# Optimization experiments

Hardware: AMD Instinct MI355X
Metric: run time of the kernel (lower is better)

The kernel has to match this reference:

```python
import jax, jax.numpy as jnp
import numpy as np

N_NODES = 50000
N_EDGES = 800000
D_IN = 256
D_OUT = 128


def setup_inputs() -> dict:
    key = jax.random.key(0)
    k1, k2, k3 = jax.random.split(key, 3)
    x = jax.random.normal(k1, (N_NODES, D_IN), dtype=jnp.float32)
    edge_index = jax.random.randint(k2, (2, N_EDGES), 0, N_NODES, dtype=jnp.int64)
    W = jax.random.normal(k3, (D_IN, D_OUT), dtype=jnp.float32) / np.sqrt(D_IN)
    b = jnp.zeros((D_OUT,), dtype=jnp.float32)
    prelu_a = jnp.full((D_OUT,), 0.25, dtype=jnp.float32)  # PyTorch PReLU default init
    return {"x": x, "edge_index": edge_index, "W": W, "b": b, "prelu_a": prelu_a}


def reference(x, edge_index, W, b, prelu_a):
    N = x.shape[0]
    # GCNConv default: add self-loops, symmetric deg^{-1/2} normalization
    self_loops = jnp.arange(N, dtype=edge_index.dtype)
    src = jnp.concatenate([edge_index[0], self_loops])  # message source j
    dst = jnp.concatenate([edge_index[1], self_loops])  # aggregation target i
    deg = jax.ops.segment_sum(jnp.ones_like(dst, dtype=x.dtype), dst, num_segments=N)
    dinv = jnp.where(deg > 0, jax.lax.rsqrt(deg), 0.0)
    norm = dinv[src] * dinv[dst]  # [E+N]
    h = x @ W  # [N, D_OUT] linear transform before aggregation
    msg = h[src] * norm[:, None]  # gather + scale
    out = jax.ops.segment_sum(msg, dst, num_segments=N) + b  # scatter-add + bias
    # per-channel PReLU
    return jnp.where(out > 0, out, prelu_a * out)
```

## Files before the change

kernel.cpp:

```cpp
#include <hip/hip_runtime.h>

#define N_NODES 50000
#define N_EDGES 800000
#define D_IN    256
#define D_OUT   128
#define ELL_S   64
#define GEMM_BLKS ((N_NODES + 127) / 128)
#define BKT_BLKS  ((N_EDGES + 1023) / 1024)
#define CNT_PAD   50176

typedef __attribute__((ext_vector_type(8))) short short8;
typedef __attribute__((ext_vector_type(4))) float floatx4;

__device__ __forceinline__ unsigned short f2bf(float f) {
    unsigned int u = __float_as_uint(f);
    unsigned int r = (u + 0x7fffu + ((u >> 16) & 1u)) >> 16;
    return (unsigned short)r;
}
__device__ __forceinline__ unsigned int pack2(float a, float b) {
    return (unsigned int)f2bf(a) | ((unsigned int)f2bf(b) << 16);
}
__device__ __forceinline__ float bfl(unsigned int u) { return __uint_as_float(u << 16); }
__device__ __forceinline__ float bfh(unsigned int u) { return __uint_as_float(u & 0xffff0000u); }

__device__ __forceinline__ int load_idx(const void* ei, int i, int is64) {
    if (is64) return (int)((const long long*)ei)[i];
    return ((const int*)ei)[i];
}

__global__ __launch_bounds__(256) void prep_kernel(const unsigned int* __restrict__ e,
                                                   int* __restrict__ is64,
                                                   const float* __restrict__ W,
                                                   unsigned short* __restrict__ bf,
                                                   int* __restrict__ cnt) {
    int bid = blockIdx.x;
    int tid = threadIdx.x;
    if (bid == 0) {
        __shared__ int found32;
        if (tid == 0) found32 = 0;
        __syncthreads();
        for (int i = tid; i < 2048; i += 256)
            if (e[2 * i + 1] != 0u) found32 = 1;
        __syncthreads();
        if (tid == 0) *is64 = (found32 ? 0 : 1);
    } else if (bid <= 16) {
        int g = (bid - 1) * 256 + tid;
        int lane = g & 63;
        int kc   = (g >> 6) & 7;
        int ct   = g >> 9;
        int n  = ct * 16 + (lane & 15);
        int kb = kc * 32 + ((lane >> 4) & 3) * 8;
        unsigned int p[4];
#pragma unroll
        for (int jj = 0; jj < 4; jj++) {
            float a = W[(size_t)(kb + 2 * jj + 0) * D_OUT + n];
            float b = W[(size_t)(kb + 2 * jj + 1) * D_OUT + n];
            p[jj] = pack2(a, b);
        }
        *(uint4*)&bf[(size_t)g * 8] = make_uint4(p[0], p[1], p[2], p[3]);
    } else {
        int i0 = ((bid - 17) * 256 + tid) * 2;
        *(int2*)&cnt[i0] = make_int2(0, 0);
    }
}

__global__ __launch_bounds__(256) void fused_kernel(const float* __restrict__ x,
                                                    const unsigned short* __restrict__ bf,
                                                    unsigned short* __restrict__ h,
                                                    const void* __restrict__ ei,
                                                    const int* __restrict__ is64p,
                                                    int* __restrict__ cnt,
                                                    int* __restrict__ bucket) {
    __shared__ unsigned short As[128][40];
    int tid = threadIdx.x;

    if (blockIdx.x >= GEMM_BLKS) {
        int base = (blockIdx.x - GEMM_BLKS) * 1024 + tid;
        int is64 = *is64p;
        int sv[4], dv[4];
        if (is64) {
            const long long* p = (const long long*)ei;
#pragma unroll
            for (int i = 0; i < 4; i++) {
                int e = base + i * 256;
                if (e < N_EDGES) { sv[i] = (int)p[e]; dv[i] = (int)p[N_EDGES + e]; }
                else { sv[i] = 0; dv[i] = -1; }
            }
        } else {
            const int* p = (const int*)ei;
#pragma unroll
            for (int i = 0; i < 4; i++) {
                int e = base + i * 256;
                if (e < N_EDGES) { sv[i] = p[e]; dv[i] = p[N_EDGES + e]; }
                else { sv[i] = 0; dv[i] = -1; }
            }
        }
        int pos[4] = {ELL_S, ELL_S, ELL_S, ELL_S};
#pragma unroll
        for (int i = 0; i < 4; i++)
            if (dv[i] >= 0) pos[i] = atomicAdd(&cnt[dv[i]], 1);
#pragma unroll
        for (int i = 0; i < 4; i++)
            if (dv[i] >= 0 && pos[i] < ELL_S) bucket[dv[i] * ELL_S + pos[i]] = sv[i];
        return;
    }

    int row0 = blockIdx.x * 128;
    int w    = tid >> 6;
    int lane = tid & 63;
    int quad = lane >> 4;
    int l15  = lane & 15;

    floatx4 acc[2][8];
#pragma unroll
    for (int i = 0; i < 2; i++)
#pragma unroll
        for (int j = 0; j < 8; j++) acc[i][j] = (floatx4){0.f, 0.f, 0.f, 0.f};

    int srow  = tid >> 1;
    int shalf = (tid & 1) * 16;
    const float* xrow = x + (size_t)(row0 + srow) * D_IN;
    bool svalid = (row0 + srow) < N_NODES;

    for (int k0 = 0; k0 < D_IN; k0 += 32) {
        uint4 p0 = make_uint4(0, 0, 0, 0), p1 = make_uint4(0, 0, 0, 0);
        if (svalid) {
            const float* src = xrow + k0 + shalf;
            float4 f0 = *(const float4*)(src + 0);
            float4 f1 = *(const float4*)(src + 4);
            float4 f2 = *(const float4*)(src + 8);
            float4 f3 = *(const float4*)(src + 12);
            p0 = make_uint4(pack2(f0.x, f0.y), pack2(f0.z, f0.w),
                            pack2(f1.x, f1.y), pack2(f1.z, f1.w));
            p1 = make_uint4(pack2(f2.x, f2.y), pack2(f2.z, f2.w),
                            pack2(f3.x, f3.y), pack2(f3.z, f3.w));
        }
        __syncthreads();
        *(uint4*)&As[srow][shalf + 0] = p0;
        *(uint4*)&As[srow][shalf + 8] = p1;
        __syncthreads();

        short8 a0 = *(const short8*)&As[w * 32 + l15][quad * 8];
        short8 a1 = *(const short8*)&As[w * 32 + 16 + l15][quad * 8];
        int kc = k0 >> 5;
#pragma unroll
        for (int ct = 0; ct < 8; ct++) {
            short8 b = *(const short8*)&bf[(size_t)(((ct * 8 + kc) * 64 + lane)) * 8];
            acc[0][ct] = __builtin_amdgcn_mfma_f32_16x16x32_bf16(a0, b, acc[0][ct], 0, 0, 0);
            acc[1][ct] = __builtin_amdgcn_mfma_f32_16x16x32_bf16(a1, b, acc[1][ct], 0, 0, 0);
        }
    }

#pragma unroll
    for (int rt = 0; rt < 2; rt++) {
        int grow0 = row0 + w * 32 + rt * 16 + quad * 4;
#pragma unroll
        for (int r = 0; r < 4; r++) {
            int grow = grow0 + r;
            if (grow < N_NODES) {
#pragma unroll
                for (int ct = 0; ct < 8; ct++) {
                    h[(size_t)grow * D_OUT + ct * 16 + l15] = f2bf(acc[rt][ct][r]);
                }
            }
        }
    }
}

#define GACC(U, F)                                      \
    a0 += bfl(U.x) * (F); a1 += bfh(U.x) * (F);         \
    a2 += bfl(U.y) * (F); a3 += bfh(U.y) * (F);         \
    a4 += bfl(U.z) * (F); a5 += bfh(U.z) * (F);         \
    a6 += bfl(U.w) * (F); a7 += bfh(U.w) * (F);

#define GBODY(SS, WW, KB)                                                         \
    {                                                                             \
        int lim = wave_max - (KB);                                                \
        if (lim > 16) lim = 16;                                                   \
        for (int k = 0; k < lim; k += 4) {                                        \
            int   s0 = __shfl((SS), gk + k + 0), s1 = __shfl((SS), gk + k + 1);   \
            int   s2 = __shfl((SS), gk + k + 2), s3 = __shfl((SS), gk + k + 3);   \
            float f0 = __shfl((WW), gk + k + 0), f1 = __shfl((WW), gk + k + 1);   \
            float f2 = __shfl((WW), gk + k + 2), f3 = __shfl((WW), gk + k + 3);   \
            uint4 u0 = *(const uint4*)(h + (size_t)s0 * D_OUT + co);              \
            uint4 u1 = *(const uint4*)(h + (size_t)s1 * D_OUT + co);              \
            uint4 u2 = *(const uint4*)(h + (size_t)s2 * D_OUT + co);              \
            uint4 u3 = *(const uint4*)(h + (size_t)s3 * D_OUT + co);              \
            GACC(u0, f0); GACC(u1, f1); GACC(u2, f2); GACC(u3, f3);               \
        }                                                                         \
    }

__global__ __launch_bounds__(256) void gather_kernel(
    const unsigned short* __restrict__ h, const int* __restrict__ cnt,
    const int* __restrict__ bucket, const float* __restrict__ bias,
    const float* __restrict__ pa, float* __restrict__ out) {
    int wave = (int)((blockIdx.x * blockDim.x + threadIdx.x) >> 6);
    int lane = threadIdx.x & 63;
    int g  = lane >> 4;
    int l  = lane & 15;
    int gk = g << 4;
    int d  = wave * 4 + g;

    int nraw = cnt[d];
    int n = nraw < ELL_S ? nraw : ELL_S;
    float di = rsqrtf((float)(nraw + 1));

    int co = l * 8;

    uint4 us = *(const uint4*)(h + (size_t)d * D_OUT + co);
    float sl = di * di;
    float a0 = bfl(us.x) * sl, a1 = bfh(us.x) * sl;
    float a2 = bfl(us.y) * sl, a3 = bfh(us.y) * sl;
    float a4 = bfl(us.z) * sl, a5 = bfh(us.z) * sl;
    float a6 = bfl(us.w) * sl, a7 = bfh(us.w) * sl;

    int db = d * ELL_S;
    int   s0v = 0,   s1v = 0,   s2v = 0,   s3v = 0;
    float w0v = 0.f, w1v = 0.f, w2v = 0.f, w3v = 0.f;
    if (l      < n) { s0v = bucket[db + l];      w0v = rsqrtf((float)(cnt[s0v] + 1)) * di; }
    if (l + 16 < n) { s1v = bucket[db + l + 16]; w1v = rsqrtf((float)(cnt[s1v] + 1)) * di; }
    if (l + 32 < n) { s2v = bucket[db + l + 32]; w2v = rsqrtf((float)(cnt[s2v] + 1)) * di; }
    if (l + 48 < n) { s3v = bucket[db + l + 48]; w3v = rsqrtf((float)(cnt[s3v] + 1)) * di; }

    int wave_max = n;
    { int t = __shfl_xor(wave_max, 16); wave_max = t > wave_max ? t : wave_max; }
    { int t = __shfl_xor(wave_max, 32); wave_max = t > wave_max ? t : wave_max; }

    if (wave_max > 0)  GBODY(s0v, w0v, 0)
    if (wave_max > 16) GBODY(s1v, w1v, 16)
    if (wave_max > 32) GBODY(s2v, w2v, 32)
    if (wave_max > 48) GBODY(s3v, w3v, 48)

    int c = l * 8;
    float4 b0 = *(const float4*)&bias[c];
    float4 b1 = *(const float4*)&bias[c + 4];
    float4 p0 = *(const float4*)&pa[c];
    float4 p1 = *(const float4*)&pa[c + 4];
    float4 o0, o1;
    o0.x = a0 + b0.x; o0.y = a1 + b0.y; o0.z = a2 + b0.z; o0.w = a3 + b0.w;
    o1.x = a4 + b1.x; o1.y = a5 + b1.y; o1.z = a6 + b1.z; o1.w = a7 + b1.w;
    o0.x = o0.x > 0.f ? o0.x : p0.x * o0.x;
    o0.y = o0.y > 0.f ? o0.y : p0.y * o0.y;
    o0.z = o0.z > 0.f ? o0.z : p0.z * o0.z;
    o0.w = o0.w > 0.f ? o0.w : p0.w * o0.w;
    o1.x = o1.x > 0.f ? o1.x : p1.x * o1.x;
    o1.y = o1.y > 0.f ? o1.y : p1.y * o1.y;
    o1.z = o1.z > 0.f ? o1.z : p1.z * o1.z;
    o1.w = o1.w > 0.f ? o1.w : p1.w * o1.w;
    *(float4*)&out[(size_t)d * D_OUT + c]     = o0;
    *(float4*)&out[(size_t)d * D_OUT + c + 4] = o1;
}

extern "C" void kernel_launch(void* const* d_in, const int* in_sizes, int n_in,
                              void* d_out, int out_size, void* d_ws, size_t ws_size,
                              hipStream_t stream) {
    const float* x  = (const float*)d_in[0];
    const void*  ei = d_in[1];
    const float* W  = (const float*)d_in[2];
    const float* b  = (const float*)d_in[3];
    const float* pa = (const float*)d_in[4];
    float* out = (float*)d_out;

    char* w = (char*)d_ws;
    int*   is64   = (int*)w;    w += 256;
    int*   cnt    = (int*)w;    w += CNT_PAD * 4;
    unsigned short* bfrag = (unsigned short*)w; w += 8 * 8 * 64 * 8 * 2;
    int*   bucket = (int*)w;    w += (size_t)N_NODES * ELL_S * 4;
    unsigned short* h = (unsigned short*)w; w += (size_t)N_NODES * D_OUT * 2;

    prep_kernel<<<1 + 16 + 98, 256, 0, stream>>>((const unsigned int*)ei, is64, W, bfrag, cnt);
    fused_kernel<<<GEMM_BLKS + BKT_BLKS, 256, 0, stream>>>(x, bfrag, h, ei, is64, cnt, bucket);
    gather_kernel<<<(N_NODES / 4 * 64 + 255) / 256, 256, 0, stream>>>(h, cnt, bucket, b, pa, out);
}
```

Before: 177.9 us.

## Partition edge bucketing by destination range across eight block bins

The edge-bucketing blocks now each read a 2048-edge chunk, and eight blocks share each chunk. Each of the eight handles only destinations inside its own eighth of the node range. The aim is to confine atomics and bucket writes per block to a smaller address range, hoping for better L2 locality and less atomic contention. The cost is that every edge is read eight times, which multiplies edge-index traffic and adds many more blocks. A guard against out-of-range waves is also added to the gather kernel.

```diff
diff --git a/kernel.cpp b/kernel.cpp
--- a/kernel.cpp
+++ b/kernel.cpp
@@ -6,8 +6,11 @@
 #define D_OUT   128
 #define ELL_S   64
 #define GEMM_BLKS ((N_NODES + 127) / 128)
-#define BKT_BLKS  ((N_EDGES + 1023) / 1024)
 #define CNT_PAD   50176
+#define NPB       (N_NODES / 8)
+#define SCHUNK    2048
+#define NCHUNK    ((N_EDGES + SCHUNK - 1) / SCHUNK)
+#define SCAT_BLKS (8 * NCHUNK)
 
 typedef __attribute__((ext_vector_type(8))) short short8;
 typedef __attribute__((ext_vector_type(4))) float floatx4;
@@ -75,33 +78,38 @@
     int tid = threadIdx.x;
 
     if (blockIdx.x >= GEMM_BLKS) {
-        int base = (blockIdx.x - GEMM_BLKS) * 1024 + tid;
+        int bin = blockIdx.x & 7;
+        int sbid = blockIdx.x - GEMM_BLKS;
+        int chunk = sbid >> 3;
+        int lo = bin * NPB, hi = lo + NPB;
         int is64 = *is64p;
-        int sv[4], dv[4];
+        int base = chunk * SCHUNK + tid;
+
+        int dv[8], sv[8];
         if (is64) {
             const long long* p = (const long long*)ei;
 #pragma unroll
-            for (int i = 0; i < 4; i++) {
+            for (int i = 0; i < 8; i++) {
                 int e = base + i * 256;
-                if (e < N_EDGES) { sv[i] = (int)p[e]; dv[i] = (int)p[N_EDGES + e]; }
-                else { sv[i] = 0; dv[i] = -1; }
+                if (e < N_EDGES) { dv[i] = (int)p[N_EDGES + e]; sv[i] = (int)p[e]; }
+                else dv[i] = -1;
             }
         } else {
             const int* p = (const int*)ei;
 #pragma unroll
-            for (int i = 0; i < 4; i++) {
+            for (int i = 0; i < 8; i++) {
                 int e = base + i * 256;
-                if (e < N_EDGES) { sv[i] = p[e]; dv[i] = p[N_EDGES + e]; }
-                else { sv[i] = 0; dv[i] = -1; }
-            }
-        }
-        int pos[4] = {ELL_S, ELL_S, ELL_S, ELL_S};
-#pragma unroll
-        for (int i = 0; i < 4; i++)
-            if (dv[i] >= 0) pos[i] = atomicAdd(&cnt[dv[i]], 1);
-#pragma unroll
-        for (int i = 0; i < 4; i++)
-            if (dv[i] >= 0 && pos[i] < ELL_S) bucket[dv[i] * ELL_S + pos[i]] = sv[i];
+                if (e < N_EDGES) { dv[i] = p[N_EDGES + e]; sv[i] = p[e]; }
+                else dv[i] = -1;
+            }
+        }
+#pragma unroll
+        for (int i = 0; i < 8; i++) {
+            if (dv[i] >= lo && dv[i] < hi) {
+                int pos = atomicAdd(&cnt[dv[i]], 1);
+                if (pos < ELL_S) bucket[dv[i] * ELL_S + pos] = sv[i];
+            }
+        }
         return;
     }
 
@@ -200,6 +208,7 @@
     int l  = lane & 15;
     int gk = g << 4;
     int d  = wave * 4 + g;
+    if (wave >= N_NODES / 4) return;
 
     int nraw = cnt[d];
     int n = nraw < ELL_S ? nraw : ELL_S;
@@ -269,6 +278,6 @@
     unsigned short* h = (unsigned short*)w; w += (size_t)N_NODES * D_OUT * 2;
 
     prep_kernel<<<1 + 16 + 98, 256, 0, stream>>>((const unsigned int*)ei, is64, W, bfrag, cnt);
-    fused_kernel<<<GEMM_BLKS + BKT_BLKS, 256, 0, stream>>>(x, bfrag, h, ei, is64, cnt, bucket);
+    fused_kernel<<<GEMM_BLKS + SCAT_BLKS, 256, 0, stream>>>(x, bfrag, h, ei, is64, cnt, bucket);
     gather_kernel<<<(N_NODES / 4 * 64 + 255) / 256, 256, 0, stream>>>(h, cnt, bucket, b, pa, out);
 }
```

Measured after the change: 170.0 us. -4.4%, faster.
